# Kernel tuning notes

Measured on AMD Instinct MI355X. Metric: run time of the kernel, lower is better.

The kernel has to match this reference:

```python
import jax, jax.numpy as jnp
import numpy as np

T, H, N, Q, C = 65536, 768, 32768, 32768, 10
MAX_LEN = 16  # max span length


def _make_spans(key, n):
    k1, k2 = jax.random.split(key)
    starts = jax.random.randint(k1, (n,), 0, T - MAX_LEN)
    lengths = jax.random.randint(k2, (n,), 1, MAX_LEN + 1)
    return jnp.stack([starts, starts + lengths], axis=1)  # [start, end)


def setup_inputs() -> dict:
    key = jax.random.key(0)
    ks = jax.random.split(key, 6)
    token_emb = jax.random.normal(ks[0], (T, H), dtype=jnp.float32)
    spans_support = _make_spans(ks[1], N)
    labels = jax.random.randint(ks[2], (N,), 0, C)
    spans_query = _make_spans(ks[3], Q)
    W_proj = jax.random.normal(ks[4], (3 * H, H), dtype=jnp.float32) * (1.0 / np.sqrt(3 * H))
    b_proj = jnp.zeros((H,), dtype=jnp.float32)
    return dict(token_emb=token_emb, spans_support=spans_support, labels=labels,
                spans_query=spans_query, W_proj=W_proj, b_proj=b_proj, n_classes=C)


def _span_embed(token_emb, spans, W, b):
    # token_emb: (T, H); spans: (n, 2) [start, end)
    s = spans[:, 0]
    e = spans[:, 1]
    # exclusive-prefix-sum trick turns per-span mean pooling into two gathers
    zero = jnp.zeros((1, token_emb.shape[1]), token_emb.dtype)
    csum = jnp.concatenate([zero, jnp.cumsum(token_emb, axis=0)], axis=0)  # (T+1, H)
    h_mean = (csum[e] - csum[s]) / (e - s).astype(token_emb.dtype)[:, None]
    feat = jnp.concatenate([token_emb[s], token_emb[e - 1], h_mean], axis=-1)  # (n, 3H)
    return jax.nn.gelu(feat @ W + b, approximate=False)  # torch nn.GELU default = erf


def _l2norm(x, eps=1e-12):
    # matches torch F.normalize: x / max(||x||, eps)
    return x / jnp.maximum(jnp.linalg.norm(x, axis=-1, keepdims=True), eps)


def reference(token_emb, spans_support, labels, spans_query, W_proj, b_proj, n_classes):
    sup = _span_embed(token_emb, spans_support, W_proj, b_proj)  # (N, H)
    qry = _span_embed(token_emb, spans_query, W_proj, b_proj)    # (Q, H)
    # prototypes = per-class mean; empty classes fall back to global mean
    sums = jax.ops.segment_sum(sup, labels, num_segments=n_classes)           # (C, H)
    counts = jax.ops.segment_sum(jnp.ones((sup.shape[0],), sup.dtype), labels,
                                 num_segments=n_classes)                       # (C,)
    gmean = sup.mean(axis=0)
    protos = jnp.where(counts[:, None] > 0,
                       sums / jnp.maximum(counts, 1.0)[:, None],
                       gmean[None, :])
    # cosine metric + constant NONE logit of 0.5
    sim = _l2norm(qry) @ _l2norm(protos).T                                     # (Q, C)
    none_logit = jnp.full((qry.shape[0], 1), 0.5, dtype=qry.dtype)
    return jnp.concatenate([sim, none_logit], axis=-1)                         # (Q, C+1)
```

## Files before the change

kernel.cpp:

```cpp
#include <hip/hip_runtime.h>
#include <stdint.h>

#define H_DIM 768
#define N_SUP 32768
#define Q_QRY 32768
#define C_CLS 10
#define M_TOT 65536
#define KG 768
#define NT 12
#define NBUCK 1024

typedef __bf16 bf16x8 __attribute__((ext_vector_type(8)));
typedef float f32x4 __attribute__((ext_vector_type(4)));
typedef __attribute__((address_space(3))) void lds_void;
typedef const __attribute__((address_space(1))) void g_void;

__device__ __forceinline__ ushort f2bf(float f) {
  union { float f; uint32_t u; } v; v.f = f;
  uint32_t r = (v.u + 0x7FFFu + ((v.u >> 16) & 1u)) >> 16;
  return (ushort)r;
}
__device__ __forceinline__ float bf2f(ushort h) {
  union { uint32_t u; float f; } v; v.u = ((uint32_t)h) << 16; return v.f;
}
__device__ __forceinline__ float gelu_f(float x) {
  return 0.5f * x * (1.0f + erff(x * 0.70710678118654752f));
}

__global__ void prep_kernel(const float* __restrict__ te, const float* __restrict__ W,
                            const int* __restrict__ spS, const int* __restrict__ spQ,
                            ushort* __restrict__ tb, ushort* __restrict__ Bt,
                            int* __restrict__ histS, int* __restrict__ histQ) {
  int b = blockIdx.x, t = threadIdx.x;
  if (b < 24576) {
    size_t i = (((size_t)b * 256) + t) * 8;
    float4 v0 = *(const float4*)(te + i);
    float4 v1 = *(const float4*)(te + i + 4);
    ushort4 o0, o1;
    o0.x = f2bf(v0.x); o0.y = f2bf(v0.y); o0.z = f2bf(v0.z); o0.w = f2bf(v0.w);
    o1.x = f2bf(v1.x); o1.y = f2bf(v1.y); o1.z = f2bf(v1.z); o1.w = f2bf(v1.w);
    *(ushort4*)(tb + i) = o0;
    *(ushort4*)(tb + i + 4) = o1;
  } else if (b < 31488) {
    int idx = (b - 24576) * 256 + t;
    int n = idx / KG, k = idx - n * KG;
    int blk = n / H_DIM;
    int c = n - blk * H_DIM;
    Bt[idx] = f2bf(W[(size_t)(blk * H_DIM + k) * H_DIM + c]);
  } else {
    __shared__ int lhS[NBUCK], lhQ[NBUCK];
    for (int i = t; i < NBUCK; i += 256) { lhS[i] = 0; lhQ[i] = 0; }
    __syncthreads();
    int b0 = b - 31488;
    for (int i = b0 * 256 + t; i < N_SUP; i += 64 * 256) {
      atomicAdd(&lhS[spS[2 * i] >> 6], 1);
      atomicAdd(&lhQ[spQ[2 * i] >> 6], 1);
    }
    __syncthreads();
    for (int i = t; i < NBUCK; i += 256) {
      if (lhS[i]) atomicAdd(&histS[i], lhS[i]);
      if (lhQ[i]) atomicAdd(&histQ[i], lhQ[i]);
    }
  }
}

__global__ void prefix2_kernel(const int* __restrict__ histS, const int* __restrict__ histQ,
                               int* __restrict__ curS, int* __restrict__ curQ) {
  __shared__ int tmp[NBUCK];
  int t = threadIdx.x;
  {
    int v = histS[t];
    tmp[t] = v;
    __syncthreads();
    for (int off = 1; off < NBUCK; off <<= 1) {
      int add = (t >= off) ? tmp[t - off] : 0;
      __syncthreads();
      tmp[t] += add;
      __syncthreads();
    }
    curS[t] = tmp[t] - v;
    __syncthreads();
  }
  {
    int v = histQ[t];
    tmp[t] = v;
    __syncthreads();
    for (int off = 1; off < NBUCK; off <<= 1) {
      int add = (t >= off) ? tmp[t - off] : 0;
      __syncthreads();
      tmp[t] += add;
      __syncthreads();
    }
    curQ[t] = tmp[t] - v;
  }
}

__global__ void scatter2_kernel(const int* __restrict__ spS, const int* __restrict__ spQ,
                                int* __restrict__ curS, int* __restrict__ curQ,
                                int2* __restrict__ sortedS, int2* __restrict__ sortedQ) {
  for (int i = blockIdx.x * 256 + threadIdx.x; i < N_SUP; i += gridDim.x * 256) {
    {
      int s = spS[2 * i], e = spS[2 * i + 1];
      int pos = atomicAdd(&curS[s >> 6], 1);
      int2 rec; rec.x = s; rec.y = (i << 5) | (e - s);
      sortedS[pos] = rec;
    }
    {
      int s = spQ[2 * i], e = spQ[2 * i + 1];
      int pos = atomicAdd(&curQ[s >> 6], 1);
      int2 rec; rec.x = s; rec.y = (i << 5) | (e - s);
      sortedQ[pos] = rec;
    }
  }
}

__global__ __launch_bounds__(512, 2) void gemm8(const ushort* __restrict__ A,
                                                const ushort* __restrict__ Bt,
                                                ushort* __restrict__ Pp,
                                                ushort* __restrict__ Qp,
                                                ushort* __restrict__ Rp) {
  __shared__ ushort lds[65536];
  char* ldsc = (char*)lds;

  int orig = blockIdx.x;
  int wg = (orig & 7) * 288 + (orig >> 3);
  int rowT = wg / 9, colT = wg - rowT * 9;
  int m0 = rowT * 256, n0 = colT * 256;

  int tid = threadIdx.x;
  int lane = tid & 63, wave = tid >> 6;
  int wr = wave >> 2, wc = wave & 3;
  int l15 = lane & 15, l4 = lane >> 4;

  int row0 = tid >> 2;
  int ss = (tid & 3) ^ ((row0 >> 1) & 3);
  size_t eA0 = (size_t)(m0 + row0) * KG + ss * 8;
  size_t eA1 = (size_t)(m0 + row0 + 128) * KG + ss * 8;
  size_t eB0 = (size_t)(n0 + row0) * KG + ss * 8;
  size_t eB1 = (size_t)(n0 + row0 + 128) * KG + ss * 8;

  int aoff[8], boff[4];
#pragma unroll
  for (int m = 0; m < 8; ++m) {
    int r = wr * 128 + m * 16 + l15;
    aoff[m] = r * 64 + ((l4 ^ ((r >> 1) & 3)) << 4);
  }
#pragma unroll
  for (int n = 0; n < 4; ++n) {
    int r = wc * 64 + n * 16 + l15;
    boff[n] = r * 64 + ((l4 ^ ((r >> 1) & 3)) << 4);
  }

  f32x4 acc[8][4];
#pragma unroll
  for (int m = 0; m < 8; ++m)
#pragma unroll
    for (int n = 0; n < 4; ++n) acc[m][n] = (f32x4){0.f, 0.f, 0.f, 0.f};

#define SLOT_A(kh, db) (ldsc + ((kh) * 2 + (db)) * 16384)
#define SLOT_B(kh, db) (ldsc + 65536 + ((kh) * 2 + (db)) * 16384)
#define STAGE_A(tk, kh, db) do { \
    char* _d = SLOT_A(kh, db) + wave * 1024; \
    size_t _k = (size_t)(tk) * 64 + (kh) * 32; \
    __builtin_amdgcn_global_load_lds((g_void*)(A + eA0 + _k), (lds_void*)_d, 16, 0, 0); \
    __builtin_amdgcn_global_load_lds((g_void*)(A + eA1 + _k), (lds_void*)(_d + 8192), 16, 0, 0); \
  } while (0)
#define STAGE_B(tk, kh, db) do { \
    char* _d = SLOT_B(kh, db) + wave * 1024; \
    size_t _k = (size_t)(tk) * 64 + (kh) * 32; \
    __builtin_amdgcn_global_load_lds((g_void*)(Bt + eB0 + _k), (lds_void*)_d, 16, 0, 0); \
    __builtin_amdgcn_global_load_lds((g_void*)(Bt + eB1 + _k), (lds_void*)(_d + 8192), 16, 0, 0); \
  } while (0)
#define LDA4(base, o) do { _Pragma("unroll") for (int m = 0; m < 4; ++m) \
    af[m] = *reinterpret_cast<const bf16x8*>((base) + aoff[(o) + m]); } while (0)
#define LDB4(base) do { _Pragma("unroll") for (int n = 0; n < 4; ++n) \
    bf[n] = *reinterpret_cast<const bf16x8*>((base) + boff[n]); } while (0)
#define MFMA_BLOCK(MB) do { _Pragma("unroll") for (int m = 0; m < 4; ++m) \
  _Pragma("unroll") for (int n = 0; n < 4; ++n) \
    acc[(MB) + m][n] = __builtin_amdgcn_mfma_f32_16x16x32_bf16(bf[n], af[m], acc[(MB) + m][n], 0, 0, 0); \
  } while (0)
#define BARX() __builtin_amdgcn_s_barrier()
#define LGKM0() asm volatile("s_waitcnt lgkmcnt(0)" ::: "memory")
#define VM8() asm volatile("s_waitcnt vmcnt(8)" ::: "memory")

  STAGE_A(0, 0, 0); STAGE_B(0, 0, 0);
  STAGE_A(0, 1, 0); STAGE_B(0, 1, 0);
  STAGE_A(1, 0, 1); STAGE_B(1, 0, 1);
  VM8();
  BARX();

  bf16x8 af[4], bf[4];
  for (int t = 0; t < NT; ++t) {
    int d = t & 1, nd = d ^ 1;
    int tk1 = (t + 1 < NT) ? t + 1 : NT - 1;
    int tk2 = (t + 2 < NT) ? t + 2 : NT - 1;
    const char* Ak0 = SLOT_A(0, d); const char* Bk0 = SLOT_B(0, d);
    const char* Ak1 = SLOT_A(1, d); const char* Bk1 = SLOT_B(1, d);
    LDA4(Ak0, 0); LDB4(Bk0);
    STAGE_A(tk1, 1, nd);
    BARX(); LGKM0();
    __builtin_amdgcn_s_setprio(1); MFMA_BLOCK(0); __builtin_amdgcn_s_setprio(0);
    BARX();
    LDA4(Ak0, 4);
    STAGE_B(tk1, 1, nd);
    BARX(); LGKM0();
    __builtin_amdgcn_s_setprio(1); MFMA_BLOCK(4); __builtin_amdgcn_s_setprio(0);
    VM8(); BARX();
    LDA4(Ak1, 0); LDB4(Bk1);
    STAGE_A(tk2, 0, d);
    BARX(); LGKM0();
    __builtin_amdgcn_s_setprio(1); MFMA_BLOCK(0); __builtin_amdgcn_s_setprio(0);
    BARX();
    LDA4(Ak1, 4);
    STAGE_B(tk2, 0, d);
    BARX(); LGKM0();
    __builtin_amdgcn_s_setprio(1); MFMA_BLOCK(4); __builtin_amdgcn_s_setprio(0);
    VM8(); BARX();
  }
  asm volatile("s_waitcnt vmcnt(0)" ::: "memory");

  {
    int plane = colT / 3;
    int pcol0 = colT * 256 - plane * 768;
    ushort* base = (plane == 0) ? Pp : ((plane == 1) ? Qp : Rp);
#pragma unroll
    for (int m = 0; m < 8; ++m) {
      int row = m0 + wr * 128 + m * 16 + l15;
#pragma unroll
      for (int n = 0; n < 4; ++n) {
        int col = pcol0 + wc * 64 + n * 16 + l4 * 4;
        uint32_t lo, hi;
        asm("v_cvt_pk_bf16_f32 %0, %1, %2" : "=v"(lo) : "v"(acc[m][n][0]), "v"(acc[m][n][1]));
        asm("v_cvt_pk_bf16_f32 %0, %1, %2" : "=v"(hi) : "v"(acc[m][n][2]), "v"(acc[m][n][3]));
        uint2 val; val.x = lo; val.y = hi;
        *reinterpret_cast<uint2*>(base + (size_t)row * H_DIM + col) = val;
      }
    }
  }
#undef SLOT_A
#undef SLOT_B
#undef STAGE_A
#undef STAGE_B
#undef LDA4
#undef LDB4
#undef MFMA_BLOCK
}

__device__ __forceinline__ void span_embed(const ushort* __restrict__ Pp,
                                           const ushort* __restrict__ Qp,
                                           const ushort* __restrict__ Rp,
                                           const float* __restrict__ bias,
                                           int s, int len, int lane, float x[3][4]) {
  int e = s + len;
  float inv = 1.0f / (float)len;
  float acc0[3][4], accr[3][4];
  const ushort* Pr = Pp + (size_t)s * H_DIM;
  const ushort* Qr = Qp + (size_t)(e - 1) * H_DIM;
#pragma unroll
  for (int c = 0; c < 3; ++c) {
    int h = c * 256 + lane * 4;
    ushort4 p = *(const ushort4*)(Pr + h);
    ushort4 q = *(const ushort4*)(Qr + h);
    acc0[c][0] = bf2f(p.x) + bf2f(q.x);
    acc0[c][1] = bf2f(p.y) + bf2f(q.y);
    acc0[c][2] = bf2f(p.z) + bf2f(q.z);
    acc0[c][3] = bf2f(p.w) + bf2f(q.w);
    accr[c][0] = accr[c][1] = accr[c][2] = accr[c][3] = 0.f;
  }
  for (int r = s; r < e; ++r) {
    const ushort* Rr = Rp + (size_t)r * H_DIM;
#pragma unroll
    for (int c = 0; c < 3; ++c) {
      int h = c * 256 + lane * 4;
      ushort4 rv = *(const ushort4*)(Rr + h);
      accr[c][0] += bf2f(rv.x); accr[c][1] += bf2f(rv.y);
      accr[c][2] += bf2f(rv.z); accr[c][3] += bf2f(rv.w);
    }
  }
#pragma unroll
  for (int c = 0; c < 3; ++c) {
    int h = c * 256 + lane * 4;
    float4 bv = *(const float4*)(bias + h);
    x[c][0] = gelu_f(acc0[c][0] + accr[c][0] * inv + bv.x);
    x[c][1] = gelu_f(acc0[c][1] + accr[c][1] * inv + bv.y);
    x[c][2] = gelu_f(acc0[c][2] + accr[c][2] * inv + bv.z);
    x[c][3] = gelu_f(acc0[c][3] + accr[c][3] * inv + bv.w);
  }
}

__global__ __launch_bounds__(256) void combine_sup(const ushort* __restrict__ Pp,
                                                   const ushort* __restrict__ Qp,
                                                   const ushort* __restrict__ Rp,
                                                   const int2* __restrict__ sortedS,
                                                   const int* __restrict__ labels,
                                                   const float* __restrict__ bias,
                                                   float* __restrict__ pSum,
                                                   float* __restrict__ pCnt) {
  __shared__ float ls[C_CLS * H_DIM];
  __shared__ int lc[C_CLS];
  int t = threadIdx.x, lane = t & 63, wave = t >> 6;
  for (int i = t; i < C_CLS * H_DIM; i += 256) ls[i] = 0.f;
  if (t < C_CLS) lc[t] = 0;
  __syncthreads();
  for (int si = wave; si < 128; si += 4) {
    int2 rec = sortedS[blockIdx.x * 128 + si];
    int s = rec.x, len = rec.y & 31, orig = rec.y >> 5;
    float x[3][4];
    span_embed(Pp, Qp, Rp, bias, s, len, lane, x);
    int lab = labels[orig];
    float* base = &ls[lab * H_DIM];
#pragma unroll
    for (int c = 0; c < 3; ++c) {
      int h = c * 256 + lane * 4;
      atomicAdd(&base[h], x[c][0]);
      atomicAdd(&base[h + 1], x[c][1]);
      atomicAdd(&base[h + 2], x[c][2]);
      atomicAdd(&base[h + 3], x[c][3]);
    }
    if (lane == 0) atomicAdd(&lc[lab], 1);
  }
  __syncthreads();
  for (int i = t; i < C_CLS * H_DIM; i += 256) atomicAdd(&pSum[i], ls[i]);
  if (t < C_CLS) atomicAdd(&pCnt[t], (float)lc[t]);
}

__global__ void proto_norm(const float* __restrict__ pSum, const float* __restrict__ pCnt,
                           float* __restrict__ pN) {
  __shared__ float red[4];
  int t = threadIdx.x, lane = t & 63, wave = t >> 6;
  for (int c = 0; c < C_CLS; ++c) {
    float cnt = pCnt[c];
    float x[3];
#pragma unroll
    for (int j = 0; j < 3; ++j) {
      int h = t + j * 256;
      float v;
      if (cnt > 0.5f) v = pSum[c * H_DIM + h] / cnt;
      else {
        float gs = 0.f;
        for (int cc = 0; cc < C_CLS; ++cc) gs += pSum[cc * H_DIM + h];
        v = gs / (float)N_SUP;
      }
      x[j] = v;
    }
    float ss = x[0] * x[0] + x[1] * x[1] + x[2] * x[2];
#pragma unroll
    for (int o = 32; o; o >>= 1) ss += __shfl_xor(ss, o);
    if (lane == 0) red[wave] = ss;
    __syncthreads();
    float tot = red[0] + red[1] + red[2] + red[3];
    float inv = 1.0f / fmaxf(sqrtf(tot), 1e-12f);
#pragma unroll
    for (int j = 0; j < 3; ++j) pN[c * H_DIM + t + j * 256] = x[j] * inv;
    __syncthreads();
  }
}

__global__ __launch_bounds__(256) void combine_qry_sim(const ushort* __restrict__ Pp,
                                                       const ushort* __restrict__ Qp,
                                                       const ushort* __restrict__ Rp,
                                                       const int2* __restrict__ sortedQ,
                                                       const float* __restrict__ bias,
                                                       const float* __restrict__ pN,
                                                       float* __restrict__ out) {
  __shared__ float lp[C_CLS * H_DIM];
  int t = threadIdx.x, lane = t & 63, wave = t >> 6;
  for (int i = t; i < C_CLS * H_DIM; i += 256) lp[i] = pN[i];
  __syncthreads();
  int2 rec = sortedQ[blockIdx.x * 4 + wave];
  int s = rec.x, len = rec.y & 31, orig = rec.y >> 5;
  float x[3][4];
  span_embed(Pp, Qp, Rp, bias, s, len, lane, x);
  float sq = 0.f;
  float dot[C_CLS];
#pragma unroll
  for (int p = 0; p < C_CLS; ++p) dot[p] = 0.f;
#pragma unroll
  for (int c = 0; c < 3; ++c) {
    int h = c * 256 + lane * 4;
    sq += x[c][0] * x[c][0] + x[c][1] * x[c][1] + x[c][2] * x[c][2] + x[c][3] * x[c][3];
#pragma unroll
    for (int p = 0; p < C_CLS; ++p) {
      float4 pv = *(const float4*)(lp + p * H_DIM + h);
      dot[p] += x[c][0] * pv.x + x[c][1] * pv.y + x[c][2] * pv.z + x[c][3] * pv.w;
    }
  }
#pragma unroll
  for (int o = 32; o; o >>= 1) {
    sq += __shfl_xor(sq, o);
#pragma unroll
    for (int p = 0; p < C_CLS; ++p) dot[p] += __shfl_xor(dot[p], o);
  }
  if (lane == 0) {
    float inv = 1.0f / fmaxf(sqrtf(sq), 1e-12f);
    float* o = out + (size_t)orig * (C_CLS + 1);
    o[0] = dot[0] * inv; o[1] = dot[1] * inv; o[2] = dot[2] * inv;
    o[3] = dot[3] * inv; o[4] = dot[4] * inv; o[5] = dot[5] * inv;
    o[6] = dot[6] * inv; o[7] = dot[7] * inv; o[8] = dot[8] * inv;
    o[9] = dot[9] * inv; o[10] = 0.5f;
  }
}

extern "C" void kernel_launch(void* const* d_in, const int* in_sizes, int n_in,
                              void* d_out, int out_size, void* d_ws, size_t ws_size,
                              hipStream_t stream) {
  const float* token_emb = (const float*)d_in[0];
  const int*   spansS    = (const int*)d_in[1];
  const int*   labels    = (const int*)d_in[2];
  const int*   spansQ    = (const int*)d_in[3];
  const float* W         = (const float*)d_in[4];
  const float* b         = (const float*)d_in[5];
  float* out = (float*)d_out;

  char* ws = (char*)d_ws;
  size_t planeB = (size_t)M_TOT * H_DIM * 2;
  ushort* Pp   = (ushort*)ws;
  ushort* Qp   = (ushort*)(ws + planeB);
  ushort* Rp   = (ushort*)(ws + 2 * planeB);
  ushort* tebf = (ushort*)(ws + 3 * planeB);
  ushort* Bt   = (ushort*)(ws + 4 * planeB);
  char*   tail = ws + 4 * planeB + (size_t)2304 * KG * 2;
  float*  pSum = (float*)tail;
  float*  pCnt = pSum + C_CLS * H_DIM;
  float*  pN   = pCnt + 64;
  int*    histS = (int*)(pN + C_CLS * H_DIM);
  int*    histQ = histS + NBUCK;
  int*    curS  = histQ + NBUCK;
  int*    curQ  = curS + NBUCK;
  int2*   sortedS = (int2*)(curQ + NBUCK);
  int2*   sortedQ = sortedS + N_SUP;

  hipMemsetAsync(pSum, 0, (C_CLS * H_DIM + 64) * sizeof(float), stream);
  hipMemsetAsync(histS, 0, 2 * NBUCK * sizeof(int), stream);
  prep_kernel<<<31552, 256, 0, stream>>>(token_emb, W, spansS, spansQ, tebf, Bt, histS, histQ);
  prefix2_kernel<<<1, NBUCK, 0, stream>>>(histS, histQ, curS, curQ);
  scatter2_kernel<<<64, 256, 0, stream>>>(spansS, spansQ, curS, curQ, sortedS, sortedQ);
  gemm8<<<2304, 512, 0, stream>>>(tebf, Bt, Pp, Qp, Rp);
  combine_sup<<<N_SUP / 128, 256, 0, stream>>>(Pp, Qp, Rp, sortedS, labels, b, pSum, pCnt);
  proto_norm<<<1, 256, 0, stream>>>(pSum, pCnt, pN);
  combine_qry_sim<<<Q_QRY / 4, 256, 0, stream>>>(Pp, Qp, Rp, sortedQ, b, pN, out);
}
```

Baseline: 716.5 us.

## Store GEMM output as interleaved PQR rows and remap combine kernel blocks

The GEMM output moves from three separate planes into one row-major (M, 2304) buffer. The MFMA operand order is swapped so that each lane writes scalar bf16 values along columns. The combine kernels now read the P/Q/R slices from the same row, and their block indices are swizzled across 8 groups (XCDs) with multiple spans per wave: combine_sup uses 256 blocks of 128 spans, and the query kernel handles 4 spans per wave with fewer blocks. The aim is better cache locality per token row and less per-block prototype LDS reload. The price is scattered 2-byte GEMM epilogue stores, which may be less efficient than the previous packed 8-byte stores.

```diff
diff --git a/kernel.cpp b/kernel.cpp
--- a/kernel.cpp
+++ b/kernel.cpp
@@ -7,6 +7,7 @@
 #define C_CLS 10
 #define M_TOT 65536
 #define KG 768
+#define NG 2304
 #define NT 12
 #define NBUCK 1024
 
@@ -116,9 +117,7 @@
 
 __global__ __launch_bounds__(512, 2) void gemm8(const ushort* __restrict__ A,
                                                 const ushort* __restrict__ Bt,
-                                                ushort* __restrict__ Pp,
-                                                ushort* __restrict__ Qp,
-                                                ushort* __restrict__ Rp) {
+                                                ushort* __restrict__ C) {
   __shared__ ushort lds[65536];
   char* ldsc = (char*)lds;
 
@@ -177,7 +176,7 @@
     bf[n] = *reinterpret_cast<const bf16x8*>((base) + boff[n]); } while (0)
 #define MFMA_BLOCK(MB) do { _Pragma("unroll") for (int m = 0; m < 4; ++m) \
   _Pragma("unroll") for (int n = 0; n < 4; ++n) \
-    acc[(MB) + m][n] = __builtin_amdgcn_mfma_f32_16x16x32_bf16(bf[n], af[m], acc[(MB) + m][n], 0, 0, 0); \
+    acc[(MB) + m][n] = __builtin_amdgcn_mfma_f32_16x16x32_bf16(af[m], bf[n], acc[(MB) + m][n], 0, 0, 0); \
   } while (0)
 #define BARX() __builtin_amdgcn_s_barrier()
 #define LGKM0() asm volatile("s_waitcnt lgkmcnt(0)" ::: "memory")
@@ -219,24 +218,16 @@
   }
   asm volatile("s_waitcnt vmcnt(0)" ::: "memory");
 
-  {
-    int plane = colT / 3;
-    int pcol0 = colT * 256 - plane * 768;
-    ushort* base = (plane == 0) ? Pp : ((plane == 1) ? Qp : Rp);
-#pragma unroll
-    for (int m = 0; m < 8; ++m) {
-      int row = m0 + wr * 128 + m * 16 + l15;
-#pragma unroll
-      for (int n = 0; n < 4; ++n) {
-        int col = pcol0 + wc * 64 + n * 16 + l4 * 4;
-        uint32_t lo, hi;
-        asm("v_cvt_pk_bf16_f32 %0, %1, %2" : "=v"(lo) : "v"(acc[m][n][0]), "v"(acc[m][n][1]));
-        asm("v_cvt_pk_bf16_f32 %0, %1, %2" : "=v"(hi) : "v"(acc[m][n][2]), "v"(acc[m][n][3]));
-        uint2 val; val.x = lo; val.y = hi;
-        *reinterpret_cast<uint2*>(base + (size_t)row * H_DIM + col) = val;
-      }
-    }
-  }
+#pragma unroll
+  for (int m = 0; m < 8; ++m)
+#pragma unroll
+    for (int n = 0; n < 4; ++n) {
+      int col = n0 + wc * 64 + n * 16 + l15;
+      size_t rb = (size_t)(m0 + wr * 128 + m * 16 + l4 * 4) * NG + col;
+#pragma unroll
+      for (int v = 0; v < 4; ++v)
+        C[rb + (size_t)v * NG] = f2bf(acc[m][n][v]);
+    }
 #undef SLOT_A
 #undef SLOT_B
 #undef STAGE_A
@@ -246,16 +237,14 @@
 #undef MFMA_BLOCK
 }
 
-__device__ __forceinline__ void span_embed(const ushort* __restrict__ Pp,
-                                           const ushort* __restrict__ Qp,
-                                           const ushort* __restrict__ Rp,
+__device__ __forceinline__ void span_embed(const ushort* __restrict__ PQR,
                                            const float* __restrict__ bias,
                                            int s, int len, int lane, float x[3][4]) {
   int e = s + len;
   float inv = 1.0f / (float)len;
   float acc0[3][4], accr[3][4];
-  const ushort* Pr = Pp + (size_t)s * H_DIM;
-  const ushort* Qr = Qp + (size_t)(e - 1) * H_DIM;
+  const ushort* Pr = PQR + (size_t)s * NG;
+  const ushort* Qr = PQR + (size_t)(e - 1) * NG + 768;
 #pragma unroll
   for (int c = 0; c < 3; ++c) {
     int h = c * 256 + lane * 4;
@@ -268,7 +257,7 @@
     accr[c][0] = accr[c][1] = accr[c][2] = accr[c][3] = 0.f;
   }
   for (int r = s; r < e; ++r) {
-    const ushort* Rr = Rp + (size_t)r * H_DIM;
+    const ushort* Rr = PQR + (size_t)r * NG + 1536;
 #pragma unroll
     for (int c = 0; c < 3; ++c) {
       int h = c * 256 + lane * 4;
@@ -288,9 +277,7 @@
   }
 }
 
-__global__ __launch_bounds__(256) void combine_sup(const ushort* __restrict__ Pp,
-                                                   const ushort* __restrict__ Qp,
-                                                   const ushort* __restrict__ Rp,
+__global__ __launch_bounds__(256) void combine_sup(const ushort* __restrict__ PQR,
                                                    const int2* __restrict__ sortedS,
                                                    const int* __restrict__ labels,
                                                    const float* __restrict__ bias,
@@ -298,24 +285,27 @@
                                                    float* __restrict__ pCnt) {
   __shared__ float ls[C_CLS * H_DIM];
   __shared__ int lc[C_CLS];
+  int b = blockIdx.x;
+  int sb = ((b & 7) << 5) + (b >> 3);
   int t = threadIdx.x, lane = t & 63, wave = t >> 6;
   for (int i = t; i < C_CLS * H_DIM; i += 256) ls[i] = 0.f;
   if (t < C_CLS) lc[t] = 0;
   __syncthreads();
-  for (int si = wave; si < 128; si += 4) {
-    int2 rec = sortedS[blockIdx.x * 128 + si];
+  for (int k = 0; k < 32; ++k) {
+    int wid = sb * 128 + wave * 32 + k;
+    int2 rec = sortedS[wid];
     int s = rec.x, len = rec.y & 31, orig = rec.y >> 5;
     float x[3][4];
-    span_embed(Pp, Qp, Rp, bias, s, len, lane, x);
+    span_embed(PQR, bias, s, len, lane, x);
     int lab = labels[orig];
-    float* base = &ls[lab * H_DIM];
+    float* basep = &ls[lab * H_DIM];
 #pragma unroll
     for (int c = 0; c < 3; ++c) {
       int h = c * 256 + lane * 4;
-      atomicAdd(&base[h], x[c][0]);
-      atomicAdd(&base[h + 1], x[c][1]);
-      atomicAdd(&base[h + 2], x[c][2]);
-      atomicAdd(&base[h + 3], x[c][3]);
+      atomicAdd(&basep[h], x[c][0]);
+      atomicAdd(&basep[h + 1], x[c][1]);
+      atomicAdd(&basep[h + 2], x[c][2]);
+      atomicAdd(&basep[h + 3], x[c][3]);
     }
     if (lane == 0) atomicAdd(&lc[lab], 1);
   }
@@ -356,48 +346,51 @@
   }
 }
 
-__global__ __launch_bounds__(256) void combine_qry_sim(const ushort* __restrict__ Pp,
-                                                       const ushort* __restrict__ Qp,
-                                                       const ushort* __restrict__ Rp,
+__global__ __launch_bounds__(256) void combine_qry_sim(const ushort* __restrict__ PQR,
                                                        const int2* __restrict__ sortedQ,
                                                        const float* __restrict__ bias,
                                                        const float* __restrict__ pN,
                                                        float* __restrict__ out) {
   __shared__ float lp[C_CLS * H_DIM];
+  int b = blockIdx.x;
+  int sb = ((b & 7) << 8) + (b >> 3);
   int t = threadIdx.x, lane = t & 63, wave = t >> 6;
   for (int i = t; i < C_CLS * H_DIM; i += 256) lp[i] = pN[i];
   __syncthreads();
-  int2 rec = sortedQ[blockIdx.x * 4 + wave];
-  int s = rec.x, len = rec.y & 31, orig = rec.y >> 5;
-  float x[3][4];
-  span_embed(Pp, Qp, Rp, bias, s, len, lane, x);
-  float sq = 0.f;
-  float dot[C_CLS];
-#pragma unroll
-  for (int p = 0; p < C_CLS; ++p) dot[p] = 0.f;
-#pragma unroll
-  for (int c = 0; c < 3; ++c) {
-    int h = c * 256 + lane * 4;
-    sq += x[c][0] * x[c][0] + x[c][1] * x[c][1] + x[c][2] * x[c][2] + x[c][3] * x[c][3];
-#pragma unroll
-    for (int p = 0; p < C_CLS; ++p) {
-      float4 pv = *(const float4*)(lp + p * H_DIM + h);
-      dot[p] += x[c][0] * pv.x + x[c][1] * pv.y + x[c][2] * pv.z + x[c][3] * pv.w;
-    }
-  }
-#pragma unroll
-  for (int o = 32; o; o >>= 1) {
-    sq += __shfl_xor(sq, o);
-#pragma unroll
-    for (int p = 0; p < C_CLS; ++p) dot[p] += __shfl_xor(dot[p], o);
-  }
-  if (lane == 0) {
-    float inv = 1.0f / fmaxf(sqrtf(sq), 1e-12f);
-    float* o = out + (size_t)orig * (C_CLS + 1);
-    o[0] = dot[0] * inv; o[1] = dot[1] * inv; o[2] = dot[2] * inv;
-    o[3] = dot[3] * inv; o[4] = dot[4] * inv; o[5] = dot[5] * inv;
-    o[6] = dot[6] * inv; o[7] = dot[7] * inv; o[8] = dot[8] * inv;
-    o[9] = dot[9] * inv; o[10] = 0.5f;
+  for (int k = 0; k < 4; ++k) {
+    int wid = sb * 16 + wave * 4 + k;
+    int2 rec = sortedQ[wid];
+    int s = rec.x, len = rec.y & 31, orig = rec.y >> 5;
+    float x[3][4];
+    span_embed(PQR, bias, s, len, lane, x);
+    float sq = 0.f;
+    float dot[C_CLS];
+#pragma unroll
+    for (int p = 0; p < C_CLS; ++p) dot[p] = 0.f;
+#pragma unroll
+    for (int c = 0; c < 3; ++c) {
+      int h = c * 256 + lane * 4;
+      sq += x[c][0] * x[c][0] + x[c][1] * x[c][1] + x[c][2] * x[c][2] + x[c][3] * x[c][3];
+#pragma unroll
+      for (int p = 0; p < C_CLS; ++p) {
+        float4 pv = *(const float4*)(lp + p * H_DIM + h);
+        dot[p] += x[c][0] * pv.x + x[c][1] * pv.y + x[c][2] * pv.z + x[c][3] * pv.w;
+      }
+    }
+#pragma unroll
+    for (int o = 32; o; o >>= 1) {
+      sq += __shfl_xor(sq, o);
+#pragma unroll
+      for (int p = 0; p < C_CLS; ++p) dot[p] += __shfl_xor(dot[p], o);
+    }
+    if (lane == 0) {
+      float inv = 1.0f / fmaxf(sqrtf(sq), 1e-12f);
+      float* o = out + (size_t)orig * (C_CLS + 1);
+      o[0] = dot[0] * inv; o[1] = dot[1] * inv; o[2] = dot[2] * inv;
+      o[3] = dot[3] * inv; o[4] = dot[4] * inv; o[5] = dot[5] * inv;
+      o[6] = dot[6] * inv; o[7] = dot[7] * inv; o[8] = dot[8] * inv;
+      o[9] = dot[9] * inv; o[10] = 0.5f;
+    }
   }
 }
 
@@ -413,13 +406,13 @@
   float* out = (float*)d_out;
 
   char* ws = (char*)d_ws;
-  size_t planeB = (size_t)M_TOT * H_DIM * 2;
-  ushort* Pp   = (ushort*)ws;
-  ushort* Qp   = (ushort*)(ws + planeB);
-  ushort* Rp   = (ushort*)(ws + 2 * planeB);
-  ushort* tebf = (ushort*)(ws + 3 * planeB);
-  ushort* Bt   = (ushort*)(ws + 4 * planeB);
-  char*   tail = ws + 4 * planeB + (size_t)2304 * KG * 2;
+  size_t pqrB = (size_t)M_TOT * NG * 2;
+  size_t tbB  = (size_t)M_TOT * H_DIM * 2;
+  size_t wtB  = (size_t)NG * KG * 2;
+  ushort* PQR  = (ushort*)ws;
+  ushort* tebf = (ushort*)(ws + pqrB);
+  ushort* Bt   = (ushort*)(ws + pqrB + tbB);
+  char*   tail = ws + pqrB + tbB + wtB;
   float*  pSum = (float*)tail;
   float*  pCnt = pSum + C_CLS * H_DIM;
   float*  pN   = pCnt + 64;
@@ -435,8 +428,8 @@
   prep_kernel<<<31552, 256, 0, stream>>>(token_emb, W, spansS, spansQ, tebf, Bt, histS, histQ);
   prefix2_kernel<<<1, NBUCK, 0, stream>>>(histS, histQ, curS, curQ);
   scatter2_kernel<<<64, 256, 0, stream>>>(spansS, spansQ, curS, curQ, sortedS, sortedQ);
-  gemm8<<<2304, 512, 0, stream>>>(tebf, Bt, Pp, Qp, Rp);
-  combine_sup<<<N_SUP / 128, 256, 0, stream>>>(Pp, Qp, Rp, sortedS, labels, b, pSum, pCnt);
+  gemm8<<<2304, 512, 0, stream>>>(tebf, Bt, PQR);
+  combine_sup<<<256, 256, 0, stream>>>(PQR, sortedS, labels, b, pSum, pCnt);
   proto_norm<<<1, 256, 0, stream>>>(pSum, pCnt, pN);
-  combine_qry_sim<<<Q_QRY / 4, 256, 0, stream>>>(Pp, Qp, Rp, sortedQ, b, pN, out);
-}
+  combine_qry_sim<<<2048, 256, 0, stream>>>(PQR, sortedQ, b, pN, out);
+}
```

Result: faster. 674.0 us (-5.9%).
